# Performance work log

Measured on AMD Instinct MI355X. Metric: run time of the kernel, lower is better.

Reference implementation:

```python
import jax, jax.numpy as jnp
import numpy as np

DMODEL = 128
HEAD = 128
SEQ = 4096
BATCH = 16

def setup_inputs() -> dict:
    key = jax.random.key(0)
    kx, kq, kk, kv = jax.random.split(key, 4)
    x = jax.random.normal(kx, (BATCH, SEQ, DMODEL), dtype=jnp.float32)
    # nn.Linear(dmodel, head_size, bias=False): store as (dmodel, head_size) so q = x @ Wq
    s = 1.0 / np.sqrt(DMODEL)
    Wq = jax.random.uniform(kq, (DMODEL, HEAD), jnp.float32, -s, s)
    Wk = jax.random.uniform(kk, (DMODEL, HEAD), jnp.float32, -s, s)
    Wv = jax.random.uniform(kv, (DMODEL, HEAD), jnp.float32, -s, s)
    return {"x": x, "Wq": Wq, "Wk": Wk, "Wv": Wv}

def reference(x, Wq, Wk, Wv):
    B, L, _ = x.shape
    scale = HEAD ** (-0.5)
    q = jnp.einsum('bld,dh->blh', x, Wq)
    k = jnp.einsum('bld,dh->blh', x, Wk)
    v = jnp.einsum('bld,dh->blh', x, Wv)
    wei = jnp.einsum('bqh,bkh->bqk', q, k) * scale  # (B, L, L)
    causal = jnp.tril(jnp.ones((L, L), dtype=bool))
    wei = jnp.where(causal, wei, -jnp.inf)
    wei = jax.nn.softmax(wei, axis=-1)
    y = jnp.einsum('bqk,bkh->bqh', wei, v)
    return y
```

## Files before the change

kernel.cpp:

```cpp
#include <hip/hip_runtime.h>
#include <hip/hip_bf16.h>
#include <stdint.h>

#define SEQ   4096
#define DM    128
#define KVB   64

typedef __attribute__((ext_vector_type(8)))  short  bf16x8;
typedef __attribute__((ext_vector_type(16))) float  f32x16;

#define SCALE_LOG2E 0.12751743f

__device__ __forceinline__ f32x16 mfma_32x32x16(bf16x8 a, bf16x8 b, f32x16 c) {
  return __builtin_amdgcn_mfma_f32_32x32x16_bf16(a, b, c, 0, 0, 0);
}

__device__ __forceinline__ void gload16(const void* g, void* l) {
  __builtin_amdgcn_global_load_lds(
      (const __attribute__((address_space(1))) unsigned int*)g,
      (__attribute__((address_space(3))) unsigned int*)l, 16, 0, 0);
}

__device__ __forceinline__ unsigned pack2bf(float a, float b) {
  float2 t; t.x = a; t.y = b;
  __hip_bfloat162 h = __float22bfloat162_rn(t);
  union { __hip_bfloat162 h2; unsigned u; } cv;
  cv.h2 = h;
  return cv.u;
}

__device__ __forceinline__ float fast_exp2(float x) {
#if defined(__has_builtin)
#if __has_builtin(__builtin_amdgcn_exp2f)
  return __builtin_amdgcn_exp2f(x);
#else
  return exp2f(x);
#endif
#else
  return exp2f(x);
#endif
}

__global__ void prep_w(const float* __restrict__ Wq, const float* __restrict__ Wk,
                       const float* __restrict__ Wv, __hip_bfloat16* __restrict__ Wb) {
  int t = blockIdx.x * 256 + threadIdx.x;
  if (t >= 12 * 8 * 64) return;
  int ct  = t >> 9;
  int rem = t & 511;
  int s   = rem >> 6;
  int l   = rem & 63;
  const float* W = (ct < 4) ? Wq : (ct < 8) ? Wk : Wv;
  float c = (ct < 4) ? SCALE_LOG2E : 1.0f;
  int h  = (ct & 3) * 32 + (l & 31);
  int d0 = 16 * s + 8 * (l >> 5);
  union { __hip_bfloat16 h8[8]; bf16x8 v; } u;
#pragma unroll
  for (int i = 0; i < 8; ++i) u.h8[i] = __float2bfloat16(W[(d0 + i) * DM + h] * c);
  *(bf16x8*)&Wb[(size_t)t * 8] = u.v;
}

__global__ void __launch_bounds__(256, 2)
proj(const float* __restrict__ x, const __hip_bfloat16* __restrict__ Wb,
     __hip_bfloat16* __restrict__ qw, __hip_bfloat16* __restrict__ kw,
     __hip_bfloat16* __restrict__ vtw) {
  __shared__ __hip_bfloat16 slab[4][1024];
  const int wave = threadIdx.x >> 6, lane = threadIdx.x & 63;
  const int l31 = lane & 31, hi = lane >> 5;
  const int t0 = blockIdx.x * 128 + wave * 32;
  const int trow = t0 + l31;

  bf16x8 af[8];
#pragma unroll
  for (int s = 0; s < 8; ++s) {
    const float* px = x + (size_t)trow * DM + 16 * s + 8 * hi;
    float4 u0 = *(const float4*)px;
    float4 u1 = *(const float4*)(px + 4);
    union { bf16x8 v; unsigned u[4]; } fr;
    fr.u[0] = pack2bf(u0.x, u0.y);
    fr.u[1] = pack2bf(u0.z, u0.w);
    fr.u[2] = pack2bf(u1.x, u1.y);
    fr.u[3] = pack2bf(u1.z, u1.w);
    af[s] = fr.v;
  }

  for (int ct = 0; ct < 12; ++ct) {
    f32x16 acc;
#pragma unroll
    for (int j = 0; j < 16; ++j) acc[j] = 0.f;
#pragma unroll
    for (int s = 0; s < 8; ++s) {
      bf16x8 bfr = *(const bf16x8*)&Wb[(size_t)((ct * 8 + s) * 64 + lane) * 8];
      acc = mfma_32x32x16(af[s], bfr, acc);
    }
    __syncthreads();
#pragma unroll
    for (int j = 0; j < 16; ++j) {
      int r = (j & 3) + 8 * (j >> 2) + 4 * hi;
      slab[wave][r * 32 + l31] = __float2bfloat16(acc[j]);
    }
    __syncthreads();
    if (ct < 8) {
      __hip_bfloat16* dst = (ct < 4) ? qw : kw;
      int hb = (ct & 3) * 32;
#pragma unroll
      for (int p = 0; p < 2; ++p) {
        int eidx = p * 512 + lane * 8;
        int tr = eidx >> 5, c = eidx & 31;
        *(bf16x8*)&dst[(size_t)(t0 + tr) * DM + hb + c] =
            *(const bf16x8*)&slab[wave][eidx];
      }
    } else {
      int d  = lane >> 1;
      int th = (lane & 1) * 16;
      int dg = (ct & 3) * 32 + d;
      int bb = t0 >> 12;
      int tl = t0 & 4095;
      __hip_bfloat16* dst = vtw + ((size_t)bb * DM + dg) * SEQ + tl + th;
#pragma unroll
      for (int k = 0; k < 4; ++k) {
        union { unsigned short u4[4]; uint2 v; } pkv;
#pragma unroll
        for (int e = 0; e < 4; ++e) {
          union { __hip_bfloat16 hh; unsigned short us; } cv;
          cv.hh = slab[wave][(th + 4 * k + e) * 32 + d];
          pkv.u4[e] = cv.us;
        }
        *(uint2*)&dst[4 * k] = pkv.v;
      }
    }
  }
}

__device__ __forceinline__ void stage_kv(const char* kb, const char* vb, int kv0,
                                         char* dst, int tid, int wave) {
  const char* ksrc = kb + (size_t)kv0 * 256;
#pragma unroll
  for (int p = 0; p < 4; ++p) {
    int lin = p * 4096 + tid * 16;
    int row = lin >> 8, cb = lin & 255;
    int so = row * 256 + (cb ^ ((row & 15) << 4));
    gload16(ksrc + so, dst + p * 4096 + (wave << 10));
  }
  const char* vsrc = vb + (size_t)kv0 * 2;
#pragma unroll
  for (int p = 0; p < 4; ++p) {
    int lin = p * 4096 + tid * 16;
    int row = lin >> 7, cb = lin & 127;
    size_t so = (size_t)row * 8192 + (size_t)(cb ^ ((row & 7) << 4));
    gload16(vsrc + so, dst + 16384 + p * 4096 + (wave << 10));
  }
}

__global__ void __launch_bounds__(256, 2)
attn(const __hip_bfloat16* __restrict__ qw, const __hip_bfloat16* __restrict__ kw,
     const __hip_bfloat16* __restrict__ vtw, float* __restrict__ out) {
  __shared__ __align__(16) char lds[65536];
  const int bid = blockIdx.x;
  const int half = bid >> 8;
  const int r8 = bid & 255;
  const int b  = r8 & 15;
  const int pp = r8 >> 4;
  const int qt = half ? (31 - pp) : pp;
  const int q0 = qt << 7;
  const int wave = threadIdx.x >> 6, lane = threadIdx.x & 63;
  const int l31 = lane & 31, hi = lane >> 5;
  const int qrow = q0 + wave * 32 + l31;
  const int tid = threadIdx.x;

  bf16x8 qf[8];
  {
    const __hip_bfloat16* qb = qw + ((size_t)b * SEQ + qrow) * DM;
#pragma unroll
    for (int s = 0; s < 8; ++s) qf[s] = *(const bf16x8*)&qb[16 * s + 8 * hi];
  }
  f32x16 yacc[4];
#pragma unroll
  for (int dt = 0; dt < 4; ++dt)
#pragma unroll
    for (int j = 0; j < 16; ++j) yacc[dt][j] = 0.f;

  float mrun = -1e30f, lsum = 0.f;
  const int nkv = 2 * qt + 2;
  const int qmaxw = q0 + wave * 32 + 31;
  const char* kb = (const char*)(kw + (size_t)b * SEQ * DM);
  const char* vb = (const char*)(vtw + (size_t)b * DM * SEQ);

  stage_kv(kb, vb, 0, lds, tid, wave);
  __syncthreads();

  for (int t = 0; t < nkv; ++t) {
    char* cur = lds + ((t & 1) << 15);
    if (t + 1 < nkv)
      stage_kv(kb, vb, (t + 1) * KVB, lds + (((t + 1) & 1) << 15), tid, wave);

    const int kv0 = t * KVB;
    if (kv0 <= qmaxw) {
      f32x16 sa, sb;
#pragma unroll
      for (int j = 0; j < 16; ++j) { sa[j] = 0.f; sb[j] = 0.f; }
#pragma unroll
      for (int s = 0; s < 8; ++s) {
        int cbs = 32 * s + 16 * hi;
        int r0 = l31, r1 = l31 + 32;
        bf16x8 k0 = *(const bf16x8*)&cur[r0 * 256 + (cbs ^ ((r0 & 15) << 4))];
        bf16x8 k1 = *(const bf16x8*)&cur[r1 * 256 + (cbs ^ ((r1 & 15) << 4))];
        sa = mfma_32x32x16(k0, qf[s], sa);
        sb = mfma_32x32x16(k1, qf[s], sb);
      }
      if (kv0 + 63 > q0 + wave * 32) {
#pragma unroll
        for (int j = 0; j < 16; ++j) {
          int rr = (j & 3) + 8 * (j >> 2) + 4 * hi;
          sa[j] = (kv0 + rr      > qrow) ? -1e30f : sa[j];
          sb[j] = (kv0 + 32 + rr > qrow) ? -1e30f : sb[j];
        }
      }
      float pmax = -1e30f;
#pragma unroll
      for (int j = 0; j < 16; ++j) pmax = fmaxf(pmax, fmaxf(sa[j], sb[j]));
      pmax = fmaxf(pmax, __shfl_xor(pmax, 32));
      if (!__all(pmax - mrun <= 8.0f)) {
        float mn = fmaxf(mrun, pmax);
        float fs = fast_exp2(mrun - mn);
        mrun = mn;
        lsum *= fs;
#pragma unroll
        for (int dt = 0; dt < 4; ++dt)
#pragma unroll
          for (int j = 0; j < 16; ++j) yacc[dt][j] *= fs;
      }
      float ps = 0.f;
#pragma unroll
      for (int j = 0; j < 16; ++j) { sa[j] = fast_exp2(sa[j] - mrun); ps += sa[j]; }
#pragma unroll
      for (int j = 0; j < 16; ++j) { sb[j] = fast_exp2(sb[j] - mrun); ps += sb[j]; }
      ps += __shfl_xor(ps, 32);
      lsum += ps;

#pragma unroll
      for (int a = 0; a < 2; ++a) {
        unsigned pk[8];
#pragma unroll
        for (int jj = 0; jj < 8; ++jj) {
          float lo  = a ? sb[2 * jj]     : sa[2 * jj];
          float hi2 = a ? sb[2 * jj + 1] : sa[2 * jj + 1];
          pk[jj] = pack2bf(lo, hi2);
        }
#pragma unroll
        for (int s2 = 0; s2 < 2; ++s2) {
          int base = 4 * s2;
          unsigned send0 = hi ? pk[base]     : pk[base + 2];
          unsigned send1 = hi ? pk[base + 1] : pk[base + 3];
          unsigned r0 = (unsigned)__shfl_xor((int)send0, 32);
          unsigned r1 = (unsigned)__shfl_xor((int)send1, 32);
          union { bf16x8 v; unsigned u[4]; } pf;
          pf.u[0] = hi ? r0 : pk[base];
          pf.u[1] = hi ? r1 : pk[base + 1];
          pf.u[2] = hi ? pk[base + 2] : r0;
          pf.u[3] = hi ? pk[base + 3] : r1;
          int cbv = 64 * a + 32 * s2 + 16 * hi;
#pragma unroll
          for (int dt = 0; dt < 4; ++dt) {
            int rv = l31 + 32 * dt;
            bf16x8 vf = *(const bf16x8*)&cur[16384 + rv * 128 + (cbv ^ ((rv & 7) << 4))];
            yacc[dt] = mfma_32x32x16(vf, pf.v, yacc[dt]);
          }
        }
      }
    }
    __syncthreads();
  }

  float inv = 1.0f / lsum;
  float* ob = out + ((size_t)b * SEQ + qrow) * DM;
#pragma unroll
  for (int dt = 0; dt < 4; ++dt) {
#pragma unroll
    for (int g = 0; g < 4; ++g) {
      float4 v;
      v.x = yacc[dt][4 * g + 0] * inv;
      v.y = yacc[dt][4 * g + 1] * inv;
      v.z = yacc[dt][4 * g + 2] * inv;
      v.w = yacc[dt][4 * g + 3] * inv;
      *(float4*)&ob[32 * dt + 8 * g + 4 * hi] = v;
    }
  }
}

extern "C" void kernel_launch(void* const* d_in, const int* in_sizes, int n_in,
                              void* d_out, int out_size, void* d_ws, size_t ws_size,
                              hipStream_t stream) {
  const float* x  = (const float*)d_in[0];
  const float* Wq = (const float*)d_in[1];
  const float* Wk = (const float*)d_in[2];
  const float* Wv = (const float*)d_in[3];
  float* out = (float*)d_out;

  char* ws = (char*)d_ws;
  __hip_bfloat16* qw  = (__hip_bfloat16*)(ws);
  __hip_bfloat16* kw  = (__hip_bfloat16*)(ws + (size_t)16 * 1024 * 1024);
  __hip_bfloat16* vtw = (__hip_bfloat16*)(ws + (size_t)32 * 1024 * 1024);
  __hip_bfloat16* Wb  = (__hip_bfloat16*)(ws + (size_t)48 * 1024 * 1024);

  prep_w<<<24, 256, 0, stream>>>(Wq, Wk, Wv, Wb);
  proj<<<512, 256, 0, stream>>>(x, Wb, qw, kw, vtw);
  attn<<<512, 256, 0, stream>>>(qw, kw, vtw, out);
}
```

Baseline: 149.0 us.

## Use 256-row query tiles with 8 waves sharing each K/V stage

Doubles the query tile to 256 rows per block, with 512 threads (8 waves), so each staged 64-row K/V chunk in LDS serves twice as many queries. It halves global K/V traffic and the number of stage operations per query. Block indexing now maps batches by bid&7, apparently to keep one batch on one XCD for L2 locality. The V LDS layout is re-swizzled to 256-byte rows so 512 threads load it in two passes. The risks are worse causal load balance, since the qt-pairing balancing is gone and tiles get lopsided, plus half as many blocks, possibly lower occupancy, and more idle waves on diagonal tiles.

```diff
diff --git a/kernel.cpp b/kernel.cpp
--- a/kernel.cpp
+++ b/kernel.cpp
@@ -135,33 +135,33 @@
                                          char* dst, int tid, int wave) {
   const char* ksrc = kb + (size_t)kv0 * 256;
 #pragma unroll
-  for (int p = 0; p < 4; ++p) {
-    int lin = p * 4096 + tid * 16;
+  for (int p = 0; p < 2; ++p) {
+    int lin = p * 8192 + tid * 16;
     int row = lin >> 8, cb = lin & 255;
-    int so = row * 256 + (cb ^ ((row & 15) << 4));
-    gload16(ksrc + so, dst + p * 4096 + (wave << 10));
+    int col = cb ^ ((row & 15) << 4);
+    gload16(ksrc + row * 256 + col, dst + p * 8192 + (wave << 10));
   }
   const char* vsrc = vb + (size_t)kv0 * 2;
 #pragma unroll
-  for (int p = 0; p < 4; ++p) {
-    int lin = p * 4096 + tid * 16;
-    int row = lin >> 7, cb = lin & 127;
-    size_t so = (size_t)row * 8192 + (size_t)(cb ^ ((row & 7) << 4));
-    gload16(vsrc + so, dst + 16384 + p * 4096 + (wave << 10));
-  }
-}
-
-__global__ void __launch_bounds__(256, 2)
+  for (int p = 0; p < 2; ++p) {
+    int lin = p * 8192 + tid * 16;
+    int row = lin >> 8, cb = lin & 255;
+    int col = cb ^ ((row & 15) << 4);
+    size_t so = (size_t)(2 * row + (col >> 7)) * 8192 + (size_t)(col & 127);
+    gload16(vsrc + so, dst + 16384 + p * 8192 + (wave << 10));
+  }
+}
+
+__global__ void __launch_bounds__(512, 2)
 attn(const __hip_bfloat16* __restrict__ qw, const __hip_bfloat16* __restrict__ kw,
      const __hip_bfloat16* __restrict__ vtw, float* __restrict__ out) {
   __shared__ __align__(16) char lds[65536];
   const int bid = blockIdx.x;
-  const int half = bid >> 8;
-  const int r8 = bid & 255;
-  const int b  = r8 & 15;
-  const int pp = r8 >> 4;
-  const int qt = half ? (31 - pp) : pp;
-  const int q0 = qt << 7;
+  const int xcd = bid & 7;
+  const int j   = bid >> 3;
+  const int b   = xcd + 8 * (j & 1);
+  const int qt  = j >> 1;
+  const int q0  = qt << 8;
   const int wave = threadIdx.x >> 6, lane = threadIdx.x & 63;
   const int l31 = lane & 31, hi = lane >> 5;
   const int qrow = q0 + wave * 32 + l31;
@@ -177,11 +177,12 @@
 #pragma unroll
   for (int dt = 0; dt < 4; ++dt)
 #pragma unroll
-    for (int j = 0; j < 16; ++j) yacc[dt][j] = 0.f;
+    for (int jj = 0; jj < 16; ++jj) yacc[dt][jj] = 0.f;
 
   float mrun = -1e30f, lsum = 0.f;
-  const int nkv = 2 * qt + 2;
-  const int qmaxw = q0 + wave * 32 + 31;
+  const int nkv = 4 * qt + 4;
+  const int qminw = q0 + wave * 32;
+  const int qmaxw = qminw + 31;
   const char* kb = (const char*)(kw + (size_t)b * SEQ * DM);
   const char* vb = (const char*)(vtw + (size_t)b * DM * SEQ);
 
@@ -197,7 +198,7 @@
     if (kv0 <= qmaxw) {
       f32x16 sa, sb;
 #pragma unroll
-      for (int j = 0; j < 16; ++j) { sa[j] = 0.f; sb[j] = 0.f; }
+      for (int jj = 0; jj < 16; ++jj) { sa[jj] = 0.f; sb[jj] = 0.f; }
 #pragma unroll
       for (int s = 0; s < 8; ++s) {
         int cbs = 32 * s + 16 * hi;
@@ -207,17 +208,17 @@
         sa = mfma_32x32x16(k0, qf[s], sa);
         sb = mfma_32x32x16(k1, qf[s], sb);
       }
-      if (kv0 + 63 > q0 + wave * 32) {
-#pragma unroll
-        for (int j = 0; j < 16; ++j) {
-          int rr = (j & 3) + 8 * (j >> 2) + 4 * hi;
-          sa[j] = (kv0 + rr      > qrow) ? -1e30f : sa[j];
-          sb[j] = (kv0 + 32 + rr > qrow) ? -1e30f : sb[j];
+      if (kv0 + 63 > qminw) {
+#pragma unroll
+        for (int jj = 0; jj < 16; ++jj) {
+          int rr = (jj & 3) + 8 * (jj >> 2) + 4 * hi;
+          sa[jj] = (kv0 + rr      > qrow) ? -1e30f : sa[jj];
+          sb[jj] = (kv0 + 32 + rr > qrow) ? -1e30f : sb[jj];
         }
       }
       float pmax = -1e30f;
 #pragma unroll
-      for (int j = 0; j < 16; ++j) pmax = fmaxf(pmax, fmaxf(sa[j], sb[j]));
+      for (int jj = 0; jj < 16; ++jj) pmax = fmaxf(pmax, fmaxf(sa[jj], sb[jj]));
       pmax = fmaxf(pmax, __shfl_xor(pmax, 32));
       if (!__all(pmax - mrun <= 8.0f)) {
         float mn = fmaxf(mrun, pmax);
@@ -227,13 +228,13 @@
 #pragma unroll
         for (int dt = 0; dt < 4; ++dt)
 #pragma unroll
-          for (int j = 0; j < 16; ++j) yacc[dt][j] *= fs;
+          for (int jj = 0; jj < 16; ++jj) yacc[dt][jj] *= fs;
       }
       float ps = 0.f;
 #pragma unroll
-      for (int j = 0; j < 16; ++j) { sa[j] = fast_exp2(sa[j] - mrun); ps += sa[j]; }
-#pragma unroll
-      for (int j = 0; j < 16; ++j) { sb[j] = fast_exp2(sb[j] - mrun); ps += sb[j]; }
+      for (int jj = 0; jj < 16; ++jj) { sa[jj] = fast_exp2(sa[jj] - mrun); ps += sa[jj]; }
+#pragma unroll
+      for (int jj = 0; jj < 16; ++jj) { sb[jj] = fast_exp2(sb[jj] - mrun); ps += sb[jj]; }
       ps += __shfl_xor(ps, 32);
       lsum += ps;
 
@@ -258,11 +259,12 @@
           pf.u[1] = hi ? r1 : pk[base + 1];
           pf.u[2] = hi ? pk[base + 2] : r0;
           pf.u[3] = hi ? pk[base + 3] : r1;
-          int cbv = 64 * a + 32 * s2 + 16 * hi;
 #pragma unroll
           for (int dt = 0; dt < 4; ++dt) {
-            int rv = l31 + 32 * dt;
-            bf16x8 vf = *(const bf16x8*)&cur[16384 + rv * 128 + (cbv ^ ((rv & 7) << 4))];
+            int vrow = (l31 >> 1) + 16 * dt;
+            int vcol = (l31 & 1) * 128 + 64 * a + 32 * s2 + 16 * hi;
+            bf16x8 vf = *(const bf16x8*)&cur[16384 + vrow * 256 +
+                                             (vcol ^ ((vrow & 15) << 4))];
             yacc[dt] = mfma_32x32x16(vf, pf.v, yacc[dt]);
           }
         }
@@ -304,5 +306,5 @@
 
   prep_w<<<24, 256, 0, stream>>>(Wq, Wk, Wv, Wb);
   proj<<<512, 256, 0, stream>>>(x, Wb, qw, kw, vtw);
-  attn<<<512, 256, 0, stream>>>(qw, kw, vtw, out);
-}
+  attn<<<256, 512, 0, stream>>>(qw, kw, vtw, out);
+}
```

Result: slower. 171.7 us (+15.3%).
